# Optimization experiments

Hardware: AMD Instinct MI355X
Metric: run time of the kernel (lower is better)

## Reference

```python
import jax, jax.numpy as jnp
import numpy as np

S = 128
E = 1024
SQRT_S = float(np.sqrt(S))
EPS = 1e-5


def rope(x):
    # x: [B, L, 2, S]; positions along dim 1, rotation over last dim.
    L = x.shape[1]
    half = x.shape[-1] // 2
    pos = jnp.arange(L, dtype=jnp.float32)
    # inv_freq = 10000 ** (arange(half)/half)  (note: increasing, as in source)
    inv_freq = jnp.power(10000.0, jnp.arange(half, dtype=jnp.float32) / half)
    sinusoid = pos[:, None, None] * inv_freq[None, None, :]  # [L,1,half]
    sin, cos = jnp.sin(sinusoid), jnp.cos(sinusoid)
    x1, x2 = jnp.split(x, 2, axis=-1)
    return jnp.concatenate([x1 * cos - x2 * sin, x2 * cos + x1 * sin], axis=-1)


def setup_inputs() -> dict:
    key = jax.random.key(0)
    ks = jax.random.split(key, 6)
    B, L, H = 4, 4096, 512
    x = jax.random.normal(ks[0], (B, L, H), dtype=jnp.float32)
    ln_w = jnp.ones((H,), jnp.float32)
    ln_b = jnp.zeros((H,), jnp.float32)
    uv_w = jax.random.normal(ks[1], (2 * E + S, H), jnp.float32) * (1.0 / np.sqrt(H))
    uv_b = jax.random.normal(ks[2], (2 * E + S,), jnp.float32) * 0.02
    gamma = jax.random.uniform(ks[3], (2, S), jnp.float32)
    beta = jax.random.uniform(ks[4], (2, S), jnp.float32)
    o_w = jax.random.normal(ks[5], (H, E), jnp.float32) * (1.0 / np.sqrt(E))
    o_b = jnp.zeros((H,), jnp.float32)
    return {"x": x, "ln_w": ln_w, "ln_b": ln_b, "uv_w": uv_w, "uv_b": uv_b,
            "gamma": gamma, "beta": beta, "o_w": o_w, "o_b": o_b}


def reference(x, ln_w, ln_b, uv_w, uv_b, gamma, beta, o_w, o_b):
    shortcut = x
    # LayerNorm
    mu = jnp.mean(x, axis=-1, keepdims=True)
    var = jnp.mean(jnp.square(x - mu), axis=-1, keepdims=True)
    xn = (x - mu) * jax.lax.rsqrt(var + EPS) * ln_w + ln_b
    # uv projection + SiLU
    uv = jax.nn.silu(xn @ uv_w.T + uv_b)  # [B,L,2E+S]
    u = uv[..., :E]
    v = uv[..., E:2 * E]
    base = uv[..., 2 * E:]  # [B,L,S]
    # gated offsets -> q,k
    base = base[:, :, None, :] * gamma[None, None] + beta  # [B,L,2,S]
    base = rope(base)
    q = base[:, :, 0, :]
    k = base[:, :, 1, :]
    # relu^2 attention
    qk = jnp.einsum('bls,bms->blm', q, k)
    kernel = jnp.square(jax.nn.relu(qk / SQRT_S))  # [B,L,L]
    out = u * jnp.einsum('blm,bme->ble', kernel, v)
    out = out @ o_w.T + o_b
    return out + shortcut
```

## Files before the change

kernel.cpp:

```cpp
#include <hip/hip_runtime.h>
#include <math.h>

#define L_DIM 4096
#define B_DIM 4
#define H_DIM 512
#define E_DIM 1024
#define S_DIM 128
#define HALF  64
#define N_ROWS 16384
#define NUV   2176
#define LN_EPS 1e-5f
#define INV_SQRT_S 0.08838834764831845f

typedef _Float16 f16;
typedef __attribute__((ext_vector_type(8))) _Float16 half8;
typedef __attribute__((ext_vector_type(4))) _Float16 half4;
typedef __attribute__((ext_vector_type(4))) float f32x4;

#define OFF_WUV  ((size_t)0)
#define OFF_WO   (OFF_WUV + 2228224)
#define OFF_U    (OFF_WO + 1048576)
#define OFF_VT   (OFF_U + 33554432)
#define OFF_AUB  (OFF_VT + 33554432)
#define OFF_Q    (OFF_AUB + 33554432)
#define OFF_K    (OFF_Q + 4194304)
#define OFF_KC0  (OFF_K + 4194304)
#define OFF_KC1  (OFF_KC0 + 33554432)
#define OFF_COS  OFF_KC1
#define OFF_SIN  (OFF_COS + 1048576)
#define OFF_XN   (OFF_SIN + 1048576)
#define OFF_BR   (OFF_XN + 16777216)

__global__ void k_tables(float* __restrict__ cosT, float* __restrict__ sinT) {
    int idx = blockIdx.x * 256 + threadIdx.x;
    if (idx >= L_DIM * HALF) return;
    int pos = idx >> 6;
    int j = idx & 63;
    float invf = (float)pow(10000.0, (double)j / 64.0);
    float angf = (float)pos * invf;
    double ang = (double)angf;
    cosT[idx] = (float)cos(ang);
    sinT[idx] = (float)sin(ang);
}

__global__ __launch_bounds__(256) void k_xn(const float* __restrict__ x,
                                            const float* __restrict__ lnw,
                                            const float* __restrict__ lnb,
                                            f16* __restrict__ xn) {
    int row = blockIdx.x * 4 + (threadIdx.x >> 6);
    int lane = threadIdx.x & 63;
    const float4* xr = (const float4*)(x + (size_t)row * H_DIM);
    float4 a = xr[lane * 2], b = xr[lane * 2 + 1];
    float s = a.x + a.y + a.z + a.w + b.x + b.y + b.z + b.w;
    float s2 = a.x * a.x + a.y * a.y + a.z * a.z + a.w * a.w
             + b.x * b.x + b.y * b.y + b.z * b.z + b.w * b.w;
#pragma unroll
    for (int off = 32; off > 0; off >>= 1) {
        s  += __shfl_xor(s, off);
        s2 += __shfl_xor(s2, off);
    }
    float m = s / (float)H_DIM;
    float var = s2 / (float)H_DIM - m * m;
    float r = rsqrtf(var + LN_EPS);
    const float4* wr4 = (const float4*)lnw;
    const float4* br4 = (const float4*)lnb;
    float4 wa = wr4[lane * 2], wb = wr4[lane * 2 + 1];
    float4 ba = br4[lane * 2], bb = br4[lane * 2 + 1];
    half8 o;
    o[0] = (f16)((a.x - m) * r * wa.x + ba.x);
    o[1] = (f16)((a.y - m) * r * wa.y + ba.y);
    o[2] = (f16)((a.z - m) * r * wa.z + ba.z);
    o[3] = (f16)((a.w - m) * r * wa.w + ba.w);
    o[4] = (f16)((b.x - m) * r * wb.x + bb.x);
    o[5] = (f16)((b.y - m) * r * wb.y + bb.y);
    o[6] = (f16)((b.z - m) * r * wb.z + bb.z);
    o[7] = (f16)((b.w - m) * r * wb.w + bb.w);
    *(half8*)(xn + (size_t)row * H_DIM + lane * 8) = o;
}

__global__ __launch_bounds__(256) void k_cvt_w(const float* __restrict__ uvw,
                                               const float* __restrict__ ow,
                                               f16* __restrict__ duv,
                                               f16* __restrict__ dow) {
    int gid = blockIdx.x * 256 + threadIdx.x;
    int i4 = gid << 2;
    const float* src;
    f16* dst;
    int off;
    if (i4 < NUV * H_DIM) { src = uvw; dst = duv; off = i4; }
    else { src = ow; dst = dow; off = i4 - NUV * H_DIM; }
    float4 v = *(const float4*)(src + off);
    half4 o = {(f16)v.x, (f16)v.y, (f16)v.z, (f16)v.w};
    *(half4*)(dst + off) = o;
}

__device__ __forceinline__ void gload16(const void* g, void* l) {
    __builtin_amdgcn_global_load_lds(
        (const __attribute__((address_space(1))) unsigned int*)g,
        (__attribute__((address_space(3))) unsigned int*)l, 16, 0, 0);
}

template <int MT, int NT>
__device__ __forceinline__ void mfma_core(const char* Ab, int lda_b,
                                          const char* Bb, int ldb_b,
                                          int K, f16* lds, f32x4 acc[MT][NT]) {
    constexpr int BM = 32 * MT, BN = 32 * NT;
    constexpr int ISS = (BM + BN) / 32;
    constexpr int ASLOTS = (BM * 128) / 1024;
    const int tid = threadIdx.x;
    const int lane = tid & 63;
    const int wv = tid >> 6;
    const int wr = wv >> 1, wc = wv & 1;
    char* ldsc = (char*)lds;

    const char* sb[ISS];
    unsigned voff[ISS];
#pragma unroll
    for (int i = 0; i < ISS; ++i) {
        const int slot = wv * ISS + i;
        const int ell = (slot << 10) + (lane << 4);
        if (slot < ASLOTS) {
            int row = ell >> 7, kb = ell & 127;
            sb[i] = Ab;
            voff[i] = (unsigned)row * (unsigned)lda_b + (unsigned)(kb ^ ((row & 7) << 4));
        } else {
            const int e2 = ell - BM * 128;
            int row = e2 >> 7, kb = e2 & 127;
            sb[i] = Bb;
            voff[i] = (unsigned)row * (unsigned)ldb_b + (unsigned)(kb ^ ((row & 7) << 4));
        }
    }
    unsigned aoff[MT], boff[NT];
#pragma unroll
    for (int mt = 0; mt < MT; ++mt) {
        int row = wr * (MT * 16) + mt * 16 + (lane & 15);
        unsigned byt = (unsigned)((row << 7) + ((lane >> 4) << 4));
        aoff[mt] = byt ^ (unsigned)((row & 7) << 4);
    }
#pragma unroll
    for (int nt = 0; nt < NT; ++nt) {
        int row = wc * (NT * 16) + nt * 16 + (lane & 15);
        unsigned byt = (unsigned)((row << 7) + ((lane >> 4) << 4));
        boff[nt] = (byt ^ (unsigned)((row & 7) << 4)) + (unsigned)(BM * 128);
    }

    for (int k0 = 0; k0 < K; k0 += 64) {
        const unsigned kbyte = (unsigned)(k0 << 1);
#pragma unroll
        for (int i = 0; i < ISS; ++i)
            gload16(sb[i] + voff[i] + kbyte, ldsc + ((wv * ISS + i) << 10));
        __syncthreads();
#pragma unroll
        for (int ks = 0; ks < 2; ++ks) {
            half8 af[MT], bf[NT];
#pragma unroll
            for (int mt = 0; mt < MT; ++mt)
                af[mt] = *(const half8*)(ldsc + (aoff[mt] ^ (unsigned)(ks << 6)));
#pragma unroll
            for (int nt = 0; nt < NT; ++nt)
                bf[nt] = *(const half8*)(ldsc + (boff[nt] ^ (unsigned)(ks << 6)));
#pragma unroll
            for (int mt = 0; mt < MT; ++mt)
#pragma unroll
                for (int nt = 0; nt < NT; ++nt)
                    acc[mt][nt] = __builtin_amdgcn_mfma_f32_16x16x32_f16(af[mt], bf[nt], acc[mt][nt], 0, 0, 0);
        }
        __syncthreads();
    }
}

__global__ __launch_bounds__(256, 4) void k_mm_uv(const f16* __restrict__ xn,
                                                  const f16* __restrict__ wuv,
                                                  const float* __restrict__ bias,
                                                  f16* __restrict__ u,
                                                  f16* __restrict__ vT,
                                                  float* __restrict__ braw) {
    __shared__ union {
        f16 stage[256 * 64];
        f16 tr[128][136];
    } sl;
    const int m0 = blockIdx.y * 128, n0 = blockIdx.x * 128;
    f32x4 acc[4][4];
#pragma unroll
    for (int i = 0; i < 4; ++i)
#pragma unroll
        for (int j = 0; j < 4; ++j) acc[i][j] = (f32x4){0.f, 0.f, 0.f, 0.f};
    mfma_core<4, 4>((const char*)(xn + (size_t)m0 * H_DIM), H_DIM * 2,
                    (const char*)(wuv + (size_t)n0 * H_DIM), H_DIM * 2,
                    H_DIM, sl.stage, acc);
    const int lane = threadIdx.x & 63, wv = threadIdx.x >> 6;
    const int wr = wv >> 1, wc = wv & 1;
    if (n0 < E_DIM) {
#pragma unroll
        for (int mt = 0; mt < 4; ++mt)
#pragma unroll
            for (int nt = 0; nt < 4; ++nt)
#pragma unroll
                for (int r = 0; r < 4; ++r) {
                    int ml = wr * 64 + mt * 16 + (lane >> 4) * 4 + r;
                    int nl = wc * 64 + nt * 16 + (lane & 15);
                    float s = acc[mt][nt][r] + bias[n0 + nl];
                    float val = s / (1.f + expf(-s));
                    u[(size_t)(m0 + ml) * E_DIM + (n0 + nl)] = (f16)val;
                }
    } else if (n0 < 2 * E_DIM) {
#pragma unroll
        for (int mt = 0; mt < 4; ++mt)
#pragma unroll
            for (int nt = 0; nt < 4; ++nt)
#pragma unroll
                for (int r = 0; r < 4; ++r) {
                    int ml = wr * 64 + mt * 16 + (lane >> 4) * 4 + r;
                    int nl = wc * 64 + nt * 16 + (lane & 15);
                    float s = acc[mt][nt][r] + bias[n0 + nl];
                    sl.tr[nl][ml] = (f16)(s / (1.f + expf(-s)));
                }
        __syncthreads();
        int rl = threadIdx.x >> 1, h = threadIdx.x & 1;
        int b = m0 >> 12;
        int mloc = m0 & (L_DIM - 1);
        size_t e = (size_t)(n0 - E_DIM) + rl;
        f16* dst = vT + ((size_t)b * E_DIM + e) * L_DIM + mloc + h * 64;
#pragma unroll
        for (int i = 0; i < 8; ++i)
            *(uint4*)(dst + i * 8) = *(const uint4*)&sl.tr[rl][h * 64 + i * 8];
    } else {
#pragma unroll
        for (int mt = 0; mt < 4; ++mt)
#pragma unroll
            for (int nt = 0; nt < 4; ++nt)
#pragma unroll
                for (int r = 0; r < 4; ++r) {
                    int ml = wr * 64 + mt * 16 + (lane >> 4) * 4 + r;
                    int nl = wc * 64 + nt * 16 + (lane & 15);
                    float s = acc[mt][nt][r] + bias[n0 + nl];
                    braw[(size_t)(m0 + ml) * S_DIM + (n0 - 2 * E_DIM + nl)] =
                        s / (1.f + expf(-s));
                }
    }
}

__global__ __launch_bounds__(256) void k_prep(const float* __restrict__ braw,
                                              const float* __restrict__ gamma,
                                              const float* __restrict__ beta,
                                              const float* __restrict__ cosT,
                                              const float* __restrict__ sinT,
                                              f16* __restrict__ q,
                                              f16* __restrict__ kq) {
    int idx = blockIdx.x * 256 + threadIdx.x;
    int row = idx >> 6;
    int j = idx & 63;
    int l = row & (L_DIM - 1);
    float b1 = braw[(size_t)row * S_DIM + j];
    float b2 = braw[(size_t)row * S_DIM + j + HALF];
    float c = cosT[l * HALF + j];
    float s = sinT[l * HALF + j];
    {
        float x1 = b1 * gamma[j] + beta[j];
        float x2 = b2 * gamma[j + HALF] + beta[j + HALF];
        q[(size_t)row * S_DIM + j] = (f16)(x1 * c - x2 * s);
        q[(size_t)row * S_DIM + j + HALF] = (f16)(x2 * c + x1 * s);
    }
    {
        float x1 = b1 * gamma[S_DIM + j] + beta[S_DIM + j];
        float x2 = b2 * gamma[S_DIM + j + HALF] + beta[S_DIM + j + HALF];
        kq[(size_t)row * S_DIM + j] = (f16)(x1 * c - x2 * s);
        kq[(size_t)row * S_DIM + j + HALF] = (f16)(x2 * c + x1 * s);
    }
}

__global__ __launch_bounds__(256) void k_mm_qk(const f16* __restrict__ q,
                                               const f16* __restrict__ k,
                                               f16* __restrict__ kc0,
                                               f16* __restrict__ kc1, int pair) {
    __shared__ f16 stage[256 * 64];
    const int b = blockIdx.z & 3;
    const int half = blockIdx.z >> 2;
    f16* kern = half ? kc1 : kc0;
    const int mc = pair * 2 + half;
    const int m0 = blockIdx.y * 128, n0 = blockIdx.x * 128;
    f32x4 acc[4][4];
#pragma unroll
    for (int i = 0; i < 4; ++i)
#pragma unroll
        for (int j = 0; j < 4; ++j) acc[i][j] = (f32x4){0.f, 0.f, 0.f, 0.f};
    const char* Ab = (const char*)(q + (size_t)(b * L_DIM + mc * 1024 + m0) * S_DIM);
    const char* Bb = (const char*)(k + (size_t)(b * L_DIM + n0) * S_DIM);
    mfma_core<4, 4>(Ab, S_DIM * 2, Bb, S_DIM * 2, S_DIM, stage, acc);
    const int lane = threadIdx.x & 63, wv = threadIdx.x >> 6;
    const int wr = wv >> 1, wc = wv & 1;
#pragma unroll
    for (int mt = 0; mt < 4; ++mt)
#pragma unroll
        for (int nt = 0; nt < 4; ++nt)
#pragma unroll
            for (int r = 0; r < 4; ++r) {
                int ml = wr * 64 + mt * 16 + (lane >> 4) * 4 + r;
                int nl = wc * 64 + nt * 16 + (lane & 15);
                float t = fmaxf(acc[mt][nt][r] * INV_SQRT_S, 0.f);
                t = fminf(t, 240.f);
                kern[(size_t)(b * 1024 + m0 + ml) * L_DIM + (n0 + nl)] = (f16)(t * t);
            }
}

__global__ __launch_bounds__(256) void k_mm_av(const f16* __restrict__ kc0,
                                               const f16* __restrict__ kc1,
                                               const f16* __restrict__ vT,
                                               const f16* __restrict__ u,
                                               f16* __restrict__ aub, int pair) {
    __shared__ union {
        f16 stage[256 * 64];
        f16 tr[128][136];
    } sl;
    const int b = blockIdx.z & 3;
    const int half = blockIdx.z >> 2;
    const f16* kern = half ? kc1 : kc0;
    const int mc = pair * 2 + half;
    const int m0 = blockIdx.x * 128, n0 = blockIdx.y * 128;
    f32x4 acc[4][4];
#pragma unroll
    for (int i = 0; i < 4; ++i)
#pragma unroll
        for (int j = 0; j < 4; ++j) acc[i][j] = (f32x4){0.f, 0.f, 0.f, 0.f};
    const char* Ab = (const char*)(kern + (size_t)(b * 1024 + m0) * L_DIM);
    const char* Bb = (const char*)(vT + ((size_t)b * E_DIM + n0) * L_DIM);
    mfma_core<4, 4>(Ab, L_DIM * 2, Bb, L_DIM * 2, L_DIM, sl.stage, acc);
    const int lane = threadIdx.x & 63, wv = threadIdx.x >> 6;
    const int wr = wv >> 1, wc = wv & 1;
#pragma unroll
    for (int nt = 0; nt < 4; ++nt) {
        int nl = wc * 64 + nt * 16 + (lane & 15);
#pragma unroll
        for (int mt = 0; mt < 4; ++mt)
#pragma unroll
            for (int r = 0; r < 4; ++r) {
                int ml = wr * 64 + mt * 16 + (lane >> 4) * 4 + r;
                sl.tr[ml][nl] = (f16)acc[mt][nt][r];
            }
    }
    __syncthreads();
    int rl = threadIdx.x >> 1, h = threadIdx.x & 1;
    size_t mg = (size_t)b * L_DIM + (size_t)mc * 1024 + m0 + rl;
    const f16* up = u + mg * E_DIM + n0 + h * 64;
    f16* ap = aub + mg * E_DIM + n0 + h * 64;
#pragma unroll
    for (int i = 0; i < 8; ++i) {
        half8 s8 = *(const half8*)&sl.tr[rl][h * 64 + i * 8];
        half8 u8 = *(const half8*)(up + i * 8);
        half8 o8;
#pragma unroll
        for (int j = 0; j < 8; ++j) {
            float val = (float)s8[j] * (float)u8[j];
            val = fminf(fmaxf(val, -60000.f), 60000.f);
            o8[j] = (f16)val;
        }
        *(half8*)(ap + i * 8) = o8;
    }
}

__global__ __launch_bounds__(256) void k_mm_out(const f16* __restrict__ aub,
                                                const f16* __restrict__ wo,
                                                const float* __restrict__ ob,
                                                const float* __restrict__ x,
                                                float* __restrict__ out) {
    __shared__ f16 stage[256 * 64];
    const int m0 = blockIdx.y * 128, n0 = blockIdx.x * 128;
    f32x4 acc[4][4];
#pragma unroll
    for (int i = 0; i < 4; ++i)
#pragma unroll
        for (int j = 0; j < 4; ++j) acc[i][j] = (f32x4){0.f, 0.f, 0.f, 0.f};
    mfma_core<4, 4>((const char*)(aub + (size_t)m0 * E_DIM), E_DIM * 2,
                    (const char*)(wo + (size_t)n0 * E_DIM), E_DIM * 2,
                    E_DIM, stage, acc);
    const int lane = threadIdx.x & 63, wv = threadIdx.x >> 6;
    const int wr = wv >> 1, wc = wv & 1;
#pragma unroll
    for (int mt = 0; mt < 4; ++mt)
#pragma unroll
        for (int nt = 0; nt < 4; ++nt)
#pragma unroll
            for (int r = 0; r < 4; ++r) {
                int ml = wr * 64 + mt * 16 + (lane >> 4) * 4 + r;
                int nl = wc * 64 + nt * 16 + (lane & 15);
                size_t m = m0 + ml;
                size_t n = n0 + nl;
                out[m * H_DIM + n] = acc[mt][nt][r] + ob[n] + x[m * H_DIM + n];
            }
}

extern "C" void kernel_launch(void* const* d_in, const int* in_sizes, int n_in,
                              void* d_out, int out_size, void* d_ws, size_t ws_size,
                              hipStream_t stream) {
    const float* x     = (const float*)d_in[0];
    const float* ln_w  = (const float*)d_in[1];
    const float* ln_b  = (const float*)d_in[2];
    const float* uv_w  = (const float*)d_in[3];
    const float* uv_b  = (const float*)d_in[4];
    const float* gamma = (const float*)d_in[5];
    const float* beta  = (const float*)d_in[6];
    const float* o_w   = (const float*)d_in[7];
    const float* o_b   = (const float*)d_in[8];
    float* out = (float*)d_out;
    char* ws = (char*)d_ws;

    f16* wuv  = (f16*)(ws + OFF_WUV);
    f16* wo   = (f16*)(ws + OFF_WO);
    f16* u    = (f16*)(ws + OFF_U);
    f16* vT   = (f16*)(ws + OFF_VT);
    f16* aub  = (f16*)(ws + OFF_AUB);
    f16* q    = (f16*)(ws + OFF_Q);
    f16* k    = (f16*)(ws + OFF_K);
    f16* kc0  = (f16*)(ws + OFF_KC0);
    f16* kc1  = (f16*)(ws + OFF_KC1);
    float* cosT = (float*)(ws + OFF_COS);
    float* sinT = (float*)(ws + OFF_SIN);
    f16* xn   = (f16*)(ws + OFF_XN);
    float* braw = (float*)(ws + OFF_BR);

    k_tables<<<1024, 256, 0, stream>>>(cosT, sinT);
    k_cvt_w<<<1600, 256, 0, stream>>>(uv_w, o_w, wuv, wo);
    k_xn<<<4096, 256, 0, stream>>>(x, ln_w, ln_b, xn);
    k_mm_uv<<<dim3(17, 128), 256, 0, stream>>>(xn, wuv, uv_b, u, vT, braw);
    k_prep<<<4096, 256, 0, stream>>>(braw, gamma, beta, cosT, sinT, q, k);
    for (int pair = 0; pair < 2; ++pair) {
        k_mm_qk<<<dim3(32, 8, 8), 256, 0, stream>>>(q, k, kc0, kc1, pair);
        k_mm_av<<<dim3(8, 8, 8), 256, 0, stream>>>(kc0, kc1, vT, u, aub, pair);
    }
    k_mm_out<<<dim3(4, 128), 256, 0, stream>>>(aub, wo, o_b, x, out);
}
```

Baseline: 357.8 us.

## Double-buffer LDS staging in attention-V and output GEMMs; fast SiLU epilogue

Adds a double-buffered variant of the MFMA main loop that issues global-to-LDS loads for the next K tile while computing on the current one, and uses it in the kernel·V and output-projection GEMMs. This aims to hide global memory latency behind MFMA work, at the cost of doubling LDS usage to 64KB per block, which may reduce occupancy. Separately, the uv projection epilogue uses an approximate exp/reciprocal SiLU, hoists bias loads, and writes u through an LDS transpose for coalesced 16-byte stores.

```diff
diff --git a/kernel.cpp b/kernel.cpp
--- a/kernel.cpp
+++ b/kernel.cpp
@@ -16,6 +16,10 @@
 typedef __attribute__((ext_vector_type(8))) _Float16 half8;
 typedef __attribute__((ext_vector_type(4))) _Float16 half4;
 typedef __attribute__((ext_vector_type(4))) float f32x4;
+
+__device__ __forceinline__ float fast_silu(float s) {
+    return s * __builtin_amdgcn_rcpf(1.f + __expf(-s));
+}
 
 #define OFF_WUV  ((size_t)0)
 #define OFF_WO   (OFF_WUV + 2228224)
@@ -169,6 +173,86 @@
     }
 }
 
+template <int MT, int NT>
+__device__ __forceinline__ void mfma_core_db(const char* Ab, int lda_b,
+                                             const char* Bb, int ldb_b,
+                                             int K, char* l0, char* l1,
+                                             f32x4 acc[MT][NT]) {
+    constexpr int BM = 32 * MT, BN = 32 * NT;
+    constexpr int ISS = (BM + BN) / 32;
+    constexpr int ASLOTS = (BM * 128) / 1024;
+    const int tid = threadIdx.x;
+    const int lane = tid & 63;
+    const int wv = tid >> 6;
+    const int wr = wv >> 1, wc = wv & 1;
+
+    const char* sb[ISS];
+    unsigned voff[ISS];
+#pragma unroll
+    for (int i = 0; i < ISS; ++i) {
+        const int slot = wv * ISS + i;
+        const int ell = (slot << 10) + (lane << 4);
+        if (slot < ASLOTS) {
+            int row = ell >> 7, kb = ell & 127;
+            sb[i] = Ab;
+            voff[i] = (unsigned)row * (unsigned)lda_b + (unsigned)(kb ^ ((row & 7) << 4));
+        } else {
+            const int e2 = ell - BM * 128;
+            int row = e2 >> 7, kb = e2 & 127;
+            sb[i] = Bb;
+            voff[i] = (unsigned)row * (unsigned)ldb_b + (unsigned)(kb ^ ((row & 7) << 4));
+        }
+    }
+    unsigned aoff[MT], boff[NT];
+#pragma unroll
+    for (int mt = 0; mt < MT; ++mt) {
+        int row = wr * (MT * 16) + mt * 16 + (lane & 15);
+        unsigned byt = (unsigned)((row << 7) + ((lane >> 4) << 4));
+        aoff[mt] = byt ^ (unsigned)((row & 7) << 4);
+    }
+#pragma unroll
+    for (int nt = 0; nt < NT; ++nt) {
+        int row = wc * (NT * 16) + nt * 16 + (lane & 15);
+        unsigned byt = (unsigned)((row << 7) + ((lane >> 4) << 4));
+        boff[nt] = (byt ^ (unsigned)((row & 7) << 4)) + (unsigned)(BM * 128);
+    }
+
+    auto stage = [&](char* dst, unsigned kbyte) {
+#pragma unroll
+        for (int i = 0; i < ISS; ++i)
+            gload16(sb[i] + voff[i] + kbyte, dst + ((wv * ISS + i) << 10));
+    };
+    auto compute = [&](const char* src) {
+#pragma unroll
+        for (int ks = 0; ks < 2; ++ks) {
+            half8 af[MT], bf[NT];
+#pragma unroll
+            for (int mt = 0; mt < MT; ++mt)
+                af[mt] = *(const half8*)(src + (aoff[mt] ^ (unsigned)(ks << 6)));
+#pragma unroll
+            for (int nt = 0; nt < NT; ++nt)
+                bf[nt] = *(const half8*)(src + (boff[nt] ^ (unsigned)(ks << 6)));
+#pragma unroll
+            for (int mt = 0; mt < MT; ++mt)
+#pragma unroll
+                for (int nt = 0; nt < NT; ++nt)
+                    acc[mt][nt] = __builtin_amdgcn_mfma_f32_16x16x32_f16(af[mt], bf[nt], acc[mt][nt], 0, 0, 0);
+        }
+    };
+
+    const int nst = K / 64;
+    stage(l0, 0u);
+    __syncthreads();
+    for (int t = 0; t < nst; t += 2) {
+        stage(l1, (unsigned)(t + 1) * 128u);
+        compute(l0);
+        __syncthreads();
+        if (t + 2 < nst) stage(l0, (unsigned)(t + 2) * 128u);
+        compute(l1);
+        __syncthreads();
+    }
+}
+
 __global__ __launch_bounds__(256, 4) void k_mm_uv(const f16* __restrict__ xn,
                                                   const f16* __restrict__ wuv,
                                                   const float* __restrict__ bias,
@@ -192,29 +276,36 @@
     const int wr = wv >> 1, wc = wv & 1;
     if (n0 < E_DIM) {
 #pragma unroll
-        for (int mt = 0; mt < 4; ++mt)
-#pragma unroll
-            for (int nt = 0; nt < 4; ++nt)
+        for (int nt = 0; nt < 4; ++nt) {
+            int nl = wc * 64 + nt * 16 + (lane & 15);
+            float bs = bias[n0 + nl];
+#pragma unroll
+            for (int mt = 0; mt < 4; ++mt)
 #pragma unroll
                 for (int r = 0; r < 4; ++r) {
                     int ml = wr * 64 + mt * 16 + (lane >> 4) * 4 + r;
-                    int nl = wc * 64 + nt * 16 + (lane & 15);
-                    float s = acc[mt][nt][r] + bias[n0 + nl];
-                    float val = s / (1.f + expf(-s));
-                    u[(size_t)(m0 + ml) * E_DIM + (n0 + nl)] = (f16)val;
+                    sl.tr[ml][nl] = (f16)fast_silu(acc[mt][nt][r] + bs);
                 }
+        }
+        __syncthreads();
+        int rl = threadIdx.x >> 1, h = threadIdx.x & 1;
+        f16* dst = u + (size_t)(m0 + rl) * E_DIM + n0 + h * 64;
+#pragma unroll
+        for (int i = 0; i < 8; ++i)
+            *(uint4*)(dst + i * 8) = *(const uint4*)&sl.tr[rl][h * 64 + i * 8];
     } else if (n0 < 2 * E_DIM) {
 #pragma unroll
-        for (int mt = 0; mt < 4; ++mt)
-#pragma unroll
-            for (int nt = 0; nt < 4; ++nt)
+        for (int nt = 0; nt < 4; ++nt) {
+            int nl = wc * 64 + nt * 16 + (lane & 15);
+            float bs = bias[n0 + nl];
+#pragma unroll
+            for (int mt = 0; mt < 4; ++mt)
 #pragma unroll
                 for (int r = 0; r < 4; ++r) {
                     int ml = wr * 64 + mt * 16 + (lane >> 4) * 4 + r;
-                    int nl = wc * 64 + nt * 16 + (lane & 15);
-                    float s = acc[mt][nt][r] + bias[n0 + nl];
-                    sl.tr[nl][ml] = (f16)(s / (1.f + expf(-s)));
+                    sl.tr[nl][ml] = (f16)fast_silu(acc[mt][nt][r] + bs);
                 }
+        }
         __syncthreads();
         int rl = threadIdx.x >> 1, h = threadIdx.x & 1;
         int b = m0 >> 12;
@@ -226,17 +317,18 @@
             *(uint4*)(dst + i * 8) = *(const uint4*)&sl.tr[rl][h * 64 + i * 8];
     } else {
 #pragma unroll
-        for (int mt = 0; mt < 4; ++mt)
-#pragma unroll
-            for (int nt = 0; nt < 4; ++nt)
+        for (int nt = 0; nt < 4; ++nt) {
+            int nl = wc * 64 + nt * 16 + (lane & 15);
+            float bs = bias[n0 + nl];
+#pragma unroll
+            for (int mt = 0; mt < 4; ++mt)
 #pragma unroll
                 for (int r = 0; r < 4; ++r) {
                     int ml = wr * 64 + mt * 16 + (lane >> 4) * 4 + r;
-                    int nl = wc * 64 + nt * 16 + (lane & 15);
-                    float s = acc[mt][nt][r] + bias[n0 + nl];
                     braw[(size_t)(m0 + ml) * S_DIM + (n0 - 2 * E_DIM + nl)] =
-                        s / (1.f + expf(-s));
+                        fast_silu(acc[mt][nt][r] + bs);
                 }
+        }
     }
 }
 
@@ -309,7 +401,7 @@
                                                const f16* __restrict__ u,
                                                f16* __restrict__ aub, int pair) {
     __shared__ union {
-        f16 stage[256 * 64];
+        struct { char s0[32768]; char s1[32768]; } st;
         f16 tr[128][136];
     } sl;
     const int b = blockIdx.z & 3;
@@ -324,7 +416,7 @@
         for (int j = 0; j < 4; ++j) acc[i][j] = (f32x4){0.f, 0.f, 0.f, 0.f};
     const char* Ab = (const char*)(kern + (size_t)(b * 1024 + m0) * L_DIM);
     const char* Bb = (const char*)(vT + ((size_t)b * E_DIM + n0) * L_DIM);
-    mfma_core<4, 4>(Ab, L_DIM * 2, Bb, L_DIM * 2, L_DIM, sl.stage, acc);
+    mfma_core_db<4, 4>(Ab, L_DIM * 2, Bb, L_DIM * 2, L_DIM, sl.st.s0, sl.st.s1, acc);
     const int lane = threadIdx.x & 63, wv = threadIdx.x >> 6;
     const int wr = wv >> 1, wc = wv & 1;
 #pragma unroll
@@ -363,30 +455,33 @@
                                                 const float* __restrict__ ob,
                                                 const float* __restrict__ x,
                                                 float* __restrict__ out) {
-    __shared__ f16 stage[256 * 64];
+    __shared__ char s0[32768];
+    __shared__ char s1[32768];
     const int m0 = blockIdx.y * 128, n0 = blockIdx.x * 128;
     f32x4 acc[4][4];
 #pragma unroll
     for (int i = 0; i < 4; ++i)
 #pragma unroll
         for (int j = 0; j < 4; ++j) acc[i][j] = (f32x4){0.f, 0.f, 0.f, 0.f};
-    mfma_core<4, 4>((const char*)(aub + (size_t)m0 * E_DIM), E_DIM * 2,
-                    (const char*)(wo + (size_t)n0 * E_DIM), E_DIM * 2,
-                    E_DIM, stage, acc);
+    mfma_core_db<4, 4>((const char*)(aub + (size_t)m0 * E_DIM), E_DIM * 2,
+                       (const char*)(wo + (size_t)n0 * E_DIM), E_DIM * 2,
+                       E_DIM, s0, s1, acc);
     const int lane = threadIdx.x & 63, wv = threadIdx.x >> 6;
     const int wr = wv >> 1, wc = wv & 1;
 #pragma unroll
-    for (int mt = 0; mt < 4; ++mt)
-#pragma unroll
-        for (int nt = 0; nt < 4; ++nt)
+    for (int nt = 0; nt < 4; ++nt) {
+        int nl = wc * 64 + nt * 16 + (lane & 15);
+        float obv = ob[n0 + nl];
+#pragma unroll
+        for (int mt = 0; mt < 4; ++mt)
 #pragma unroll
             for (int r = 0; r < 4; ++r) {
                 int ml = wr * 64 + mt * 16 + (lane >> 4) * 4 + r;
-                int nl = wc * 64 + nt * 16 + (lane & 15);
                 size_t m = m0 + ml;
                 size_t n = n0 + nl;
-                out[m * H_DIM + n] = acc[mt][nt][r] + ob[n] + x[m * H_DIM + n];
+                out[m * H_DIM + n] = acc[mt][nt][r] + obv + x[m * H_DIM + n];
             }
+    }
 }
 
 extern "C" void kernel_launch(void* const* d_in, const int* in_sizes, int n_in,
```

New measurement: 328.9 us. -8.1%, faster.
